# Performance work log

Measured on AMD Instinct MI355X. Metric: run time of the kernel, lower is better.

Reference implementation:

```python
import jax, jax.numpy as jnp
import numpy as np

IN_C = 256
OUT_C = 256
QK_C = OUT_C // 8  # channel_reduction_rate = 8
B, H, W = 8, 64, 64


def setup_inputs() -> dict:
    key = jax.random.key(0)
    ks = jax.random.split(key, 7)
    s_in = 1.0 / np.sqrt(IN_C)  # torch Conv2d default init scale (kernel=1)
    return {
        "x": jax.random.normal(ks[0], (B, IN_C, H, W), dtype=jnp.float32),
        "W1": jax.random.uniform(ks[1], (OUT_C, IN_C), jnp.float32, -s_in, s_in),
        "b1": jax.random.uniform(ks[2], (OUT_C,), jnp.float32, -s_in, s_in),
        "W2": jax.random.uniform(ks[3], (QK_C, IN_C), jnp.float32, -s_in, s_in),
        "b2": jax.random.uniform(ks[4], (QK_C,), jnp.float32, -s_in, s_in),
        "W3": jax.random.uniform(ks[5], (QK_C, IN_C), jnp.float32, -s_in, s_in),
        "b3": jax.random.uniform(ks[6], (QK_C,), jnp.float32, -s_in, s_in),
    }


def reference(x, W1, b1, W2, b2, W3, b3):
    b, c, h, w = x.shape
    n = h * w
    xf = x.reshape(b, c, n)  # 1x1 conv == channel matmul on flattened spatial
    v = jnp.einsum("oc,bcn->bon", W1, xf) + b1[None, :, None]   # [B, OUT_C, N]
    q = jnp.einsum("oc,bcn->bon", W2, xf) + b2[None, :, None]   # [B, QK_C, N]
    k = jnp.einsum("oc,bcn->bon", W3, xf) + b3[None, :, None]   # [B, QK_C, N]
    scores = jnp.einsum("bdn,bdm->bnm", q, k)                    # [B, N, N]
    # GLOBAL softmax over the full flattened NxN matrix per batch element
    attn = jax.nn.softmax(scores.reshape(b, -1), axis=1).reshape(b, n, n)
    out = jnp.einsum("bon,bnm->bom", v, attn)                    # [B, OUT_C, N]
    return out.reshape(x.shape) + x
```

## Files before the change

kernel.cpp:

```cpp
#include <hip/hip_runtime.h>
#include <math.h>

#define NBATCH 8
#define NC 256
#define ND 32
#define SN 4096

constexpr size_t VB_B   = 0;
constexpr size_t QT_B   = 16777216;
constexpr size_t KT_B   = QT_B + 2097152;
constexpr size_t PM_B   = KT_B + 2097152;
constexpr size_t PS_B   = PM_B + 32768;
constexpr size_t C_B    = PS_B + 32768;
constexpr size_t WB_B   = C_B + 64;
constexpr size_t BIAS_B = WB_B + 163840;

typedef __attribute__((ext_vector_type(8))) short short8;
typedef __attribute__((ext_vector_type(4))) float f32x4;

__device__ __forceinline__ unsigned bf16rne(float f) {
  unsigned u = __float_as_uint(f);
  return (u + 0x7fffu + ((u >> 16) & 1u)) >> 16;
}
__device__ __forceinline__ unsigned bfpack(float lo, float hi) {
  return bf16rne(lo) | (bf16rne(hi) << 16);
}

__global__ __launch_bounds__(256) void prep_kernel(
    const float* __restrict__ W1, const float* __restrict__ b1,
    const float* __restrict__ W2, const float* __restrict__ b2,
    const float* __restrict__ W3, const float* __restrict__ b3,
    char* __restrict__ wsb)
{
  ushort* Wb = (ushort*)(wsb + WB_B);
  float* bias = (float*)(wsb + BIAS_B);
  const float LOG2E = 1.4426950408889634f;
  int idx = blockIdx.x * 256 + threadIdx.x;
  int r = idx >> 6, c4 = (idx & 63) * 4;
  float4 v; float sc = 1.0f;
  if (r < 256)      { v = *(const float4*)(W1 + (size_t)r * 256 + c4); }
  else if (r < 288) { v = *(const float4*)(W2 + (size_t)(r - 256) * 256 + c4); sc = LOG2E; }
  else              { v = *(const float4*)(W3 + (size_t)(r - 288) * 256 + c4); }
  ushort4 o;
  o.x = (ushort)bf16rne(v.x * sc); o.y = (ushort)bf16rne(v.y * sc);
  o.z = (ushort)bf16rne(v.z * sc); o.w = (ushort)bf16rne(v.w * sc);
  *(ushort4*)(Wb + (size_t)r * 256 + c4) = o;
  if (blockIdx.x == 0 && threadIdx.x < 320) {
    int q = threadIdx.x;
    bias[q] = q < 256 ? b1[q] : (q < 288 ? b2[q - 256] * LOG2E : b3[q - 288]);
  }
}

__global__ __launch_bounds__(512) void proj_kernel(
    const float* __restrict__ x, char* __restrict__ wsb)
{
  __shared__ alignas(16) char xT[65536];
  __shared__ alignas(16) char Wsh[40960];
  const int bid = blockIdx.x;
  const int b = bid & 7, nt = bid >> 3;
  const int n0 = nt * 128;
  const int t = threadIdx.x, w = t >> 6, lane = t & 63;
  const int l4 = lane >> 4, l16 = lane & 15;
  const float* xb = x + (size_t)b * NC * SN;
  const ushort* Wb = (const ushort*)(wsb + WB_B);
  const float* bias = (const float*)(wsb + BIAS_B);
  ushort* vbuf  = (ushort*)(wsb + VB_B);
  ushort* qtbuf = (ushort*)(wsb + QT_B);
  ushort* ktbuf = (ushort*)(wsb + KT_B);

  {
    int cp = w * 16 + l16;
    int c  = cp * 2;
    int nb0 = l4 * 4;
#pragma unroll
    for (int ni = 0; ni < 8; ++ni) {
      int nB = ni * 16 + nb0;
      float4 a0 = *(const float4*)(xb + (size_t)c * SN + n0 + nB);
      float4 a1 = *(const float4*)(xb + (size_t)(c + 1) * SN + n0 + nB);
      const float* p0 = (const float*)&a0;
      const float* p1 = (const float*)&a1;
#pragma unroll
      for (int j = 0; j < 4; ++j) {
        int n = nB + j;
        *(uint*)(xT + n * 512 + ((cp * 4) ^ ((n & 7) << 4))) = bfpack(p0[j], p1[j]);
      }
    }
  }
#pragma unroll
  for (int ii = 0; ii < 5; ++ii) {
    int slot = t + ii * 512;
    int r = slot >> 3, cc = slot & 7;
    *(uint4*)(Wsh + r * 128 + ((cc * 16) ^ ((r & 7) << 4))) =
        *(const uint4*)(Wb + (size_t)r * 256 + cc * 8);
  }
  __syncthreads();

  const int of_g = w >> 1;
  const int nf_g = w & 1;
  f32x4 acc[5][4] = {};

  for (int c4 = 0; c4 < 4; ++c4) {
#pragma unroll
    for (int kk = 0; kk < 2; ++kk) {
      short8 a[4];
#pragma unroll
      for (int nf = 0; nf < 4; ++nf) {
        int n = nf_g * 64 + nf * 16 + l16;
        a[nf] = *(const short8*)(xT + n * 512 +
                 ((c4 * 128 + kk * 64 + l4 * 16) ^ ((n & 7) << 4)));
      }
#pragma unroll
      for (int of = 0; of < 5; ++of) {
        int o = (of_g * 5 + of) * 16 + l16;
        short8 bf = *(const short8*)(Wsh + o * 128 +
                    ((kk * 64 + l4 * 16) ^ ((o & 7) << 4)));
#pragma unroll
        for (int nf = 0; nf < 4; ++nf)
          acc[of][nf] = __builtin_amdgcn_mfma_f32_16x16x32_bf16(a[nf], bf, acc[of][nf], 0, 0, 0);
      }
    }
    if (c4 < 3) {
      __syncthreads();
#pragma unroll
      for (int ii = 0; ii < 5; ++ii) {
        int slot = t + ii * 512;
        int r = slot >> 3, cc = slot & 7;
        *(uint4*)(Wsh + r * 128 + ((cc * 16) ^ ((r & 7) << 4))) =
            *(const uint4*)(Wb + (size_t)r * 256 + (c4 + 1) * 64 + cc * 8);
      }
      __syncthreads();
    }
  }

#pragma unroll
  for (int of = 0; of < 5; ++of) {
    int o = (of_g * 5 + of) * 16 + l16;
    float bv = bias[o];
#pragma unroll
    for (int nf = 0; nf < 4; ++nf) {
      int nb = nf_g * 64 + nf * 16 + l4 * 4;
      float v0 = acc[of][nf][0] + bv, v1 = acc[of][nf][1] + bv;
      float v2 = acc[of][nf][2] + bv, v3 = acc[of][nf][3] + bv;
      if (o < 256) {
        uint2 pk; pk.x = bfpack(v0, v1); pk.y = bfpack(v2, v3);
        *(uint2*)(vbuf + ((size_t)b * NC + o) * SN + n0 + nb) = pk;
      } else if (o < 288) {
        int d = o - 256;
        qtbuf[((size_t)b * SN + n0 + nb + 0) * ND + d] = (ushort)bf16rne(v0);
        qtbuf[((size_t)b * SN + n0 + nb + 1) * ND + d] = (ushort)bf16rne(v1);
        qtbuf[((size_t)b * SN + n0 + nb + 2) * ND + d] = (ushort)bf16rne(v2);
        qtbuf[((size_t)b * SN + n0 + nb + 3) * ND + d] = (ushort)bf16rne(v3);
      } else {
        int d = o - 288;
        ktbuf[((size_t)b * SN + n0 + nb + 0) * ND + d] = (ushort)bf16rne(v0);
        ktbuf[((size_t)b * SN + n0 + nb + 1) * ND + d] = (ushort)bf16rne(v1);
        ktbuf[((size_t)b * SN + n0 + nb + 2) * ND + d] = (ushort)bf16rne(v2);
        ktbuf[((size_t)b * SN + n0 + nb + 3) * ND + d] = (ushort)bf16rne(v3);
      }
    }
  }
}

__global__ __launch_bounds__(256) void qk_stats(
    const char* __restrict__ wsb, float* __restrict__ pm, float* __restrict__ ps)
{
  __shared__ alignas(16) char qt_s[128 * 64];
  __shared__ alignas(16) char kt_s[128 * 64];
  __shared__ float wm[4], wz[4];
  const int bid = blockIdx.x;
  const int b = bid & 7, ny = (bid >> 3) & 31, mx = bid >> 8;
  const int n0 = ny * 128, m0 = mx * 128;
  const int t = threadIdx.x, w = t >> 6, lane = t & 63;
  const int l4 = lane >> 4, l16 = lane & 15;
  const ushort* qtb = (const ushort*)(wsb + QT_B) + (size_t)b * SN * ND;
  const ushort* ktb = (const ushort*)(wsb + KT_B) + (size_t)b * SN * ND;
  {
    int row = t >> 1, db = (t & 1) * 32;
#pragma unroll
    for (int i = 0; i < 2; ++i) {
      int b16 = db + i * 16;
      int dst = row * 64 + (b16 ^ ((row & 3) << 4));
      *(uint4*)(qt_s + dst) = *(const uint4*)(qtb + (size_t)(n0 + row) * ND + b16 / 2);
      *(uint4*)(kt_s + dst) = *(const uint4*)(ktb + (size_t)(m0 + row) * ND + b16 / 2);
    }
  }
  __syncthreads();
  const f32x4 zf = {0.f, 0.f, 0.f, 0.f};
  short8 bfr[2];
#pragma unroll
  for (int j = 0; j < 2; ++j) {
    int mm = (w * 2 + j) * 16 + l16;
    bfr[j] = *(const short8*)(kt_s + mm * 64 + ((l4 * 16) ^ ((mm & 3) << 4)));
  }
  f32x4 sfr[8][2];
#pragma unroll
  for (int i = 0; i < 8; ++i) {
    int nn = i * 16 + l16;
    short8 af = *(const short8*)(qt_s + nn * 64 + ((l4 * 16) ^ ((nn & 3) << 4)));
#pragma unroll
    for (int j = 0; j < 2; ++j)
      sfr[i][j] = __builtin_amdgcn_mfma_f32_16x16x32_bf16(af, bfr[j], zf, 0, 0, 0);
  }
  float mt = -1e30f;
#pragma unroll
  for (int i = 0; i < 8; ++i)
#pragma unroll
    for (int j = 0; j < 2; ++j)
#pragma unroll
      for (int r = 0; r < 4; ++r) mt = fmaxf(mt, sfr[i][j][r]);
  float zt = 0.f;
#pragma unroll
  for (int i = 0; i < 8; ++i)
#pragma unroll
    for (int j = 0; j < 2; ++j)
#pragma unroll
      for (int r = 0; r < 4; ++r) zt += exp2f(sfr[i][j][r] - mt);

#pragma unroll
  for (int off = 1; off < 64; off <<= 1) {
    float m2 = __shfl_xor(mt, off);
    float z2 = __shfl_xor(zt, off);
    float M = fmaxf(mt, m2);
    zt = zt * exp2f(mt - M) + z2 * exp2f(m2 - M);
    mt = M;
  }
  if (lane == 0) { wm[w] = mt; wz[w] = zt; }
  __syncthreads();
  if (t == 0) {
    float m = wm[0], z = wz[0];
#pragma unroll
    for (int i = 1; i < 4; ++i) {
      float M = fmaxf(m, wm[i]);
      z = z * exp2f(m - M) + wz[i] * exp2f(wm[i] - M);
      m = M;
    }
    int idx = (b * 32 + ny) * 32 + mx;
    pm[idx] = m; ps[idx] = z;
  }
}

__global__ __launch_bounds__(256) void reduce_kernel(char* __restrict__ wsb)
{
  const int b = blockIdx.x;
  const float* pm = (const float*)(wsb + PM_B) + (size_t)b * 1024;
  const float* ps = (const float*)(wsb + PS_B) + (size_t)b * 1024;
  const int t = threadIdx.x;
  float m = -1e30f, z = 0.f;
  for (int i = t; i < 1024; i += 256) {
    float m2 = pm[i], z2 = ps[i];
    float M = fmaxf(m, m2);
    z = z * exp2f(m - M) + z2 * exp2f(m2 - M);
    m = M;
  }
#pragma unroll
  for (int off = 1; off < 64; off <<= 1) {
    float m2 = __shfl_xor(m, off);
    float z2 = __shfl_xor(z, off);
    float M = fmaxf(m, m2);
    z = z * exp2f(m - M) + z2 * exp2f(m2 - M);
    m = M;
  }
  __shared__ float wm[4], wz[4];
  int w = t >> 6;
  if ((t & 63) == 0) { wm[w] = m; wz[w] = z; }
  __syncthreads();
  if (t == 0) {
    float M = wm[0], Z = wz[0];
#pragma unroll
    for (int i = 1; i < 4; ++i) {
      float Mn = fmaxf(M, wm[i]);
      Z = Z * exp2f(M - Mn) + wz[i] * exp2f(wm[i] - Mn);
      M = Mn;
    }
    ((float*)(wsb + C_B))[b] = M + log2f(Z);
  }
}

__global__ __launch_bounds__(512) void attn_out(
    const char* __restrict__ wsb, const float* __restrict__ x, float* __restrict__ out)
{
  __shared__ alignas(16) char kt_s[16384];
  __shared__ alignas(16) char qt_s[2][4096];
  __shared__ alignas(16) char as_s[2][32768];
  const int bid = blockIdx.x;
  const int b = bid & 7, mt = bid >> 3;
  const int m0 = mt * 128;
  const int t = threadIdx.x, w = t >> 6, lane = t & 63;
  const int l4 = lane >> 4, l16 = lane & 15;
  const ushort* vb  = (const ushort*)(wsb + VB_B) + (size_t)b * NC * SN;
  const ushort* qtb = (const ushort*)(wsb + QT_B) + (size_t)b * SN * ND;
  const ushort* ktb = (const ushort*)(wsb + KT_B) + (size_t)b * SN * ND;
  const float Cb = ((const float*)(wsb + C_B))[b];

  {
    int row = t >> 2, sl = t & 3;
    *(uint4*)(kt_s + row * 64 + ((sl * 16) ^ ((row & 3) << 4))) =
        *(const uint4*)(ktb + (size_t)(m0 + row) * ND + sl * 8);
  }
  const int qrow = t >> 3, qsl = t & 7;
  *(uint2*)(qt_s[0] + qrow * 64 + ((qsl * 8) ^ ((qrow & 3) << 4))) =
      *(const uint2*)(qtb + (size_t)qrow * ND + qsl * 4);
  __syncthreads();

  const int mS = w * 16 + l16;
  short8 bfr = *(const short8*)(kt_s + mS * 64 + ((l4 * 16) ^ ((mS & 3) << 4)));

  const int o_q = (w >> 1) * 64;
  const int m_h = (w & 1) * 64;
  const f32x4 zf = {0.f, 0.f, 0.f, 0.f};
  f32x4 acc[4][4] = {};
  int cur = 0;

  for (int i = 0; i < 64; ++i) {
    const int n0 = i * 64;
    short8 vf[2][4];
#pragma unroll
    for (int kk = 0; kk < 2; ++kk)
#pragma unroll
      for (int of = 0; of < 4; ++of)
        vf[kk][of] = *(const short8*)(vb + (size_t)(o_q + of * 16 + l16) * SN +
                                      n0 + kk * 32 + l4 * 8);
    uint2 qnext;
    const bool pf = (i < 63);
    if (pf) qnext = *(const uint2*)(qtb + (size_t)(n0 + 64 + qrow) * ND + qsl * 4);

    {
      short8 afr[4];
#pragma unroll
      for (int nf = 0; nf < 4; ++nf) {
        int n = nf * 16 + l16;
        afr[nf] = *(const short8*)(qt_s[cur] + n * 64 + ((l4 * 16) ^ ((n & 3) << 4)));
      }
#pragma unroll
      for (int nf = 0; nf < 4; ++nf) {
        f32x4 sv = __builtin_amdgcn_mfma_f32_16x16x32_bf16(afr[nf], bfr, zf, 0, 0, 0);
        uint2 pk;
        pk.x = bfpack(exp2f(sv[0] - Cb), exp2f(sv[1] - Cb));
        pk.y = bfpack(exp2f(sv[2] - Cb), exp2f(sv[3] - Cb));
        int nb2 = (nf * 16 + l4 * 4) * 2;
        *(uint2*)(as_s[cur] + mS * 256 + (nb2 ^ ((mS & 7) << 4))) = pk;
      }
    }
    if (pf)
      *(uint2*)(qt_s[cur ^ 1] + qrow * 64 + ((qsl * 8) ^ ((qrow & 3) << 4))) = qnext;
    __syncthreads();

#pragma unroll
    for (int kk = 0; kk < 2; ++kk) {
#pragma unroll
      for (int mf = 0; mf < 4; ++mf) {
        int m = m_h + mf * 16 + l16;
        short8 af = *(const short8*)(as_s[cur] + m * 256 +
                     ((kk * 64 + l4 * 16) ^ ((m & 7) << 4)));
#pragma unroll
        for (int of = 0; of < 4; ++of)
          acc[of][mf] = __builtin_amdgcn_mfma_f32_16x16x32_bf16(vf[kk][of], af, acc[of][mf], 0, 0, 0);
      }
    }
    cur ^= 1;
  }

#pragma unroll
  for (int of = 0; of < 4; ++of)
#pragma unroll
    for (int mf = 0; mf < 4; ++mf) {
      int mg = m0 + m_h + mf * 16 + l16;
#pragma unroll
      for (int j = 0; j < 4; ++j) {
        int o = o_q + of * 16 + l4 * 4 + j;
        size_t idx = ((size_t)b * NC + o) * SN + mg;
        out[idx] = acc[of][mf][j] + x[idx];
      }
    }
}

extern "C" void kernel_launch(void* const* d_in, const int* in_sizes, int n_in,
                              void* d_out, int out_size, void* d_ws, size_t ws_size,
                              hipStream_t stream)
{
  const float* x  = (const float*)d_in[0];
  const float* W1 = (const float*)d_in[1];
  const float* b1 = (const float*)d_in[2];
  const float* W2 = (const float*)d_in[3];
  const float* b2 = (const float*)d_in[4];
  const float* W3 = (const float*)d_in[5];
  const float* b3 = (const float*)d_in[6];
  char* wsb  = (char*)d_ws;
  float* out = (float*)d_out;

  prep_kernel<<<80, 256, 0, stream>>>(W1, b1, W2, b2, W3, b3, wsb);
  proj_kernel<<<256, 512, 0, stream>>>(x, wsb);
  qk_stats<<<8192, 256, 0, stream>>>(wsb, (float*)(wsb + PM_B), (float*)(wsb + PS_B));
  reduce_kernel<<<NBATCH, 256, 0, stream>>>(wsb);
  attn_out<<<256, 512, 0, stream>>>(wsb, x, out);
}
```

Baseline: 236.0 us.

## Retile attn_out to 64-column tiles with 128-row n steps and more blocks

The attention-output kernel now processes 64 output columns per block instead of 128 and launches 512 blocks. Each iteration covers 128 n positions, with each wave owning 32 output channels across all 64 columns, and shared memory per block is roughly halved. The goal is more resident blocks per CU and better occupancy, with s_setprio raised around the MFMA loop. It also swaps the manual bf16 rounding for the HIP intrinsic conversion. The trade-off is that V is re-read from global memory twice as often across blocks, and the exp work is redistributed.

```diff
diff --git a/kernel.cpp b/kernel.cpp
--- a/kernel.cpp
+++ b/kernel.cpp
@@ -1,4 +1,5 @@
 #include <hip/hip_runtime.h>
+#include <hip/hip_bf16.h>
 #include <math.h>
 
 #define NBATCH 8
@@ -22,8 +23,11 @@
   unsigned u = __float_as_uint(f);
   return (u + 0x7fffu + ((u >> 16) & 1u)) >> 16;
 }
-__device__ __forceinline__ unsigned bfpack(float lo, float hi) {
-  return bf16rne(lo) | (bf16rne(hi) << 16);
+__device__ __forceinline__ unsigned bfpack2(float lo, float hi) {
+  union { __hip_bfloat162 h; unsigned u; } cv;
+  cv.h.x = __float2bfloat16(lo);
+  cv.h.y = __float2bfloat16(hi);
+  return cv.u;
 }
 
 __global__ __launch_bounds__(256) void prep_kernel(
@@ -42,8 +46,8 @@
   else if (r < 288) { v = *(const float4*)(W2 + (size_t)(r - 256) * 256 + c4); sc = LOG2E; }
   else              { v = *(const float4*)(W3 + (size_t)(r - 288) * 256 + c4); }
   ushort4 o;
-  o.x = (ushort)bf16rne(v.x * sc); o.y = (ushort)bf16rne(v.y * sc);
-  o.z = (ushort)bf16rne(v.z * sc); o.w = (ushort)bf16rne(v.w * sc);
+  o.x = (ushort)bfpack2(v.x * sc, 0.f); o.y = (ushort)bfpack2(v.y * sc, 0.f);
+  o.z = (ushort)bfpack2(v.z * sc, 0.f); o.w = (ushort)bfpack2(v.w * sc, 0.f);
   *(ushort4*)(Wb + (size_t)r * 256 + c4) = o;
   if (blockIdx.x == 0 && threadIdx.x < 320) {
     int q = threadIdx.x;
@@ -82,7 +86,7 @@
 #pragma unroll
       for (int j = 0; j < 4; ++j) {
         int n = nB + j;
-        *(uint*)(xT + n * 512 + ((cp * 4) ^ ((n & 7) << 4))) = bfpack(p0[j], p1[j]);
+        *(uint*)(xT + n * 512 + ((cp * 4) ^ ((n & 7) << 4))) = bfpack2(p0[j], p1[j]);
       }
     }
   }
@@ -142,7 +146,7 @@
       float v0 = acc[of][nf][0] + bv, v1 = acc[of][nf][1] + bv;
       float v2 = acc[of][nf][2] + bv, v3 = acc[of][nf][3] + bv;
       if (o < 256) {
-        uint2 pk; pk.x = bfpack(v0, v1); pk.y = bfpack(v2, v3);
+        uint2 pk; pk.x = bfpack2(v0, v1); pk.y = bfpack2(v2, v3);
         *(uint2*)(vbuf + ((size_t)b * NC + o) * SN + n0 + nb) = pk;
       } else if (o < 288) {
         int d = o - 256;
@@ -276,15 +280,15 @@
   }
 }
 
-__global__ __launch_bounds__(512) void attn_out(
+__global__ __launch_bounds__(512, 4) void attn_out(
     const char* __restrict__ wsb, const float* __restrict__ x, float* __restrict__ out)
 {
-  __shared__ alignas(16) char kt_s[16384];
-  __shared__ alignas(16) char qt_s[2][4096];
-  __shared__ alignas(16) char as_s[2][32768];
+  __shared__ alignas(16) char kt_s[4096];
+  __shared__ alignas(16) char qt_s[2][8192];
+  __shared__ alignas(16) char as_s[2][16384];
   const int bid = blockIdx.x;
   const int b = bid & 7, mt = bid >> 3;
-  const int m0 = mt * 128;
+  const int m0 = mt * 64;
   const int t = threadIdx.x, w = t >> 6, lane = t & 63;
   const int l4 = lane >> 4, l16 = lane & 15;
   const ushort* vb  = (const ushort*)(wsb + VB_B) + (size_t)b * NC * SN;
@@ -292,83 +296,80 @@
   const ushort* ktb = (const ushort*)(wsb + KT_B) + (size_t)b * SN * ND;
   const float Cb = ((const float*)(wsb + C_B))[b];
 
-  {
+  if (t < 256) {
     int row = t >> 2, sl = t & 3;
     *(uint4*)(kt_s + row * 64 + ((sl * 16) ^ ((row & 3) << 4))) =
         *(const uint4*)(ktb + (size_t)(m0 + row) * ND + sl * 8);
   }
-  const int qrow = t >> 3, qsl = t & 7;
-  *(uint2*)(qt_s[0] + qrow * 64 + ((qsl * 8) ^ ((qrow & 3) << 4))) =
-      *(const uint2*)(qtb + (size_t)qrow * ND + qsl * 4);
-  __syncthreads();
-
-  const int mS = w * 16 + l16;
+  const int qrow = t >> 2, qsl = t & 3;
+  *(uint4*)(qt_s[0] + qrow * 64 + ((qsl * 16) ^ ((qrow & 3) << 4))) =
+      *(const uint4*)(qtb + (size_t)qrow * ND + qsl * 8);
+  __syncthreads();
+
+  const int mS = (w & 3) * 16 + l16;
+  const int nh_s = w >> 2;
   short8 bfr = *(const short8*)(kt_s + mS * 64 + ((l4 * 16) ^ ((mS & 3) << 4)));
 
-  const int o_q = (w >> 1) * 64;
-  const int m_h = (w & 1) * 64;
+  const ushort* vp0 = vb + (size_t)(w * 32 + l16) * SN + l4 * 8;
+  const ushort* vp1 = vp0 + (size_t)16 * SN;
+
   const f32x4 zf = {0.f, 0.f, 0.f, 0.f};
-  f32x4 acc[4][4] = {};
+  f32x4 acc[2][4] = {};
   int cur = 0;
 
-  for (int i = 0; i < 64; ++i) {
-    const int n0 = i * 64;
+  for (int i = 0; i < 32; ++i) {
     short8 vf[2][4];
 #pragma unroll
-    for (int kk = 0; kk < 2; ++kk)
-#pragma unroll
-      for (int of = 0; of < 4; ++of)
-        vf[kk][of] = *(const short8*)(vb + (size_t)(o_q + of * 16 + l16) * SN +
-                                      n0 + kk * 32 + l4 * 8);
-    uint2 qnext;
-    const bool pf = (i < 63);
-    if (pf) qnext = *(const uint2*)(qtb + (size_t)(n0 + 64 + qrow) * ND + qsl * 4);
-
-    {
-      short8 afr[4];
-#pragma unroll
-      for (int nf = 0; nf < 4; ++nf) {
-        int n = nf * 16 + l16;
-        afr[nf] = *(const short8*)(qt_s[cur] + n * 64 + ((l4 * 16) ^ ((n & 3) << 4)));
-      }
-#pragma unroll
-      for (int nf = 0; nf < 4; ++nf) {
-        f32x4 sv = __builtin_amdgcn_mfma_f32_16x16x32_bf16(afr[nf], bfr, zf, 0, 0, 0);
-        uint2 pk;
-        pk.x = bfpack(exp2f(sv[0] - Cb), exp2f(sv[1] - Cb));
-        pk.y = bfpack(exp2f(sv[2] - Cb), exp2f(sv[3] - Cb));
-        int nb2 = (nf * 16 + l4 * 4) * 2;
-        *(uint2*)(as_s[cur] + mS * 256 + (nb2 ^ ((mS & 7) << 4))) = pk;
-      }
+    for (int kk = 0; kk < 4; ++kk) {
+      vf[0][kk] = *(const short8*)(vp0 + kk * 32);
+      vf[1][kk] = *(const short8*)(vp1 + kk * 32);
+    }
+    vp0 += 128; vp1 += 128;
+    uint4 qnext;
+    const bool pf = (i < 31);
+    if (pf) qnext = *(const uint4*)(qtb + (size_t)((i + 1) * 128 + qrow) * ND + qsl * 8);
+
+#pragma unroll
+    for (int ii = 0; ii < 4; ++ii) {
+      int nf = nh_s * 4 + ii;
+      int n = nf * 16 + l16;
+      short8 af = *(const short8*)(qt_s[cur] + n * 64 + ((l4 * 16) ^ ((n & 3) << 4)));
+      f32x4 sv = __builtin_amdgcn_mfma_f32_16x16x32_bf16(af, bfr, zf, 0, 0, 0);
+      uint2 pk;
+      pk.x = bfpack2(exp2f(sv[0] - Cb), exp2f(sv[1] - Cb));
+      pk.y = bfpack2(exp2f(sv[2] - Cb), exp2f(sv[3] - Cb));
+      int nb2 = (nf * 16 + l4 * 4) * 2;
+      *(uint2*)(as_s[cur] + mS * 256 + (nb2 ^ ((mS & 7) << 4))) = pk;
     }
     if (pf)
-      *(uint2*)(qt_s[cur ^ 1] + qrow * 64 + ((qsl * 8) ^ ((qrow & 3) << 4))) = qnext;
+      *(uint4*)(qt_s[cur ^ 1] + qrow * 64 + ((qsl * 16) ^ ((qrow & 3) << 4))) = qnext;
     __syncthreads();
 
-#pragma unroll
-    for (int kk = 0; kk < 2; ++kk) {
+    __builtin_amdgcn_s_setprio(1);
+#pragma unroll
+    for (int kk = 0; kk < 4; ++kk) {
 #pragma unroll
       for (int mf = 0; mf < 4; ++mf) {
-        int m = m_h + mf * 16 + l16;
-        short8 af = *(const short8*)(as_s[cur] + m * 256 +
-                     ((kk * 64 + l4 * 16) ^ ((m & 7) << 4)));
-#pragma unroll
-        for (int of = 0; of < 4; ++of)
-          acc[of][mf] = __builtin_amdgcn_mfma_f32_16x16x32_bf16(vf[kk][of], af, acc[of][mf], 0, 0, 0);
-      }
-    }
+        int m = mf * 16 + l16;
+        short8 paf = *(const short8*)(as_s[cur] + m * 256 +
+                      ((kk * 64 + l4 * 16) ^ ((m & 7) << 4)));
+        acc[0][mf] = __builtin_amdgcn_mfma_f32_16x16x32_bf16(vf[0][kk], paf, acc[0][mf], 0, 0, 0);
+        acc[1][mf] = __builtin_amdgcn_mfma_f32_16x16x32_bf16(vf[1][kk], paf, acc[1][mf], 0, 0, 0);
+      }
+    }
+    __builtin_amdgcn_s_setprio(0);
     cur ^= 1;
   }
 
 #pragma unroll
-  for (int of = 0; of < 4; ++of)
+  for (int of = 0; of < 2; ++of)
 #pragma unroll
     for (int mf = 0; mf < 4; ++mf) {
-      int mg = m0 + m_h + mf * 16 + l16;
+      int m = m0 + mf * 16 + l16;
 #pragma unroll
       for (int j = 0; j < 4; ++j) {
-        int o = o_q + of * 16 + l4 * 4 + j;
-        size_t idx = ((size_t)b * NC + o) * SN + mg;
+        int o = w * 32 + of * 16 + l4 * 4 + j;
+        size_t idx = ((size_t)b * NC + o) * SN + m;
         out[idx] = acc[of][mf][j] + x[idx];
       }
     }
@@ -392,5 +393,5 @@
   proj_kernel<<<256, 512, 0, stream>>>(x, wsb);
   qk_stats<<<8192, 256, 0, stream>>>(wsb, (float*)(wsb + PM_B), (float*)(wsb + PS_B));
   reduce_kernel<<<NBATCH, 256, 0, stream>>>(wsb);
-  attn_out<<<256, 512, 0, stream>>>(wsb, x, out);
-}
+  attn_out<<<512, 512, 0, stream>>>(wsb, x, out);
+}
```

Measured after the change: 210.6 us. 10.8% less time.
